# Performance work log

Measured on AMD Instinct MI355X. Metric: run time of the kernel, lower is better.

The kernel has to match this reference:

```python
import jax, jax.numpy as jnp
import numpy as np

N, E, D, H = 50000, 800000, 128, 8
HD = D // H
EPS = 1e-5


def _layernorm(x, w, b):
    # Custom LayerNorm from the repo: divides by (unbiased std + eps), not sqrt(var+eps)
    mu = x.mean(axis=-1, keepdims=True)
    sd = x.std(axis=-1, keepdims=True, ddof=1)
    return (x - mu) / (sd + EPS) * w + b


def setup_inputs() -> dict:
    key = jax.random.key(0)
    ks = jax.random.split(key, 16)
    s = 1.0 / np.sqrt(D)
    inp = {
        "feats": jax.random.normal(ks[0], (N, D), jnp.float32),
        "edge_index": jax.random.randint(ks[1], (E, 2), 0, N, jnp.int32),
        "Wq": jax.random.normal(ks[2], (D, D), jnp.float32) * s,
        "bq": jnp.zeros((D,), jnp.float32),
        "Wk": jax.random.normal(ks[3], (D, D), jnp.float32) * s,
        "bk": jnp.zeros((D,), jnp.float32),
        "Wv": jax.random.normal(ks[4], (D, D), jnp.float32) * s,
        "bv": jnp.zeros((D,), jnp.float32),
        "Wo": jax.random.normal(ks[5], (D, D), jnp.float32) * s,
        "bo": jnp.zeros((D,), jnp.float32),
        "ln1_w": jnp.ones((D,), jnp.float32),
        "ln1_b": jnp.zeros((D,), jnp.float32),
        "ln2_w": jnp.ones((D,), jnp.float32),
        "ln2_b": jnp.zeros((D,), jnp.float32),
        "W1": jax.random.normal(ks[6], (4 * D, D), jnp.float32) * s,
        "b1": jnp.zeros((4 * D,), jnp.float32),
        "W2": jax.random.normal(ks[7], (D, 4 * D), jnp.float32) * (1.0 / np.sqrt(4 * D)),
        "b2": jnp.zeros((D,), jnp.float32),
    }
    return inp


def reference(feats, edge_index, Wq, bq, Wk, bk, Wv, bv, Wo, bo,
              ln1_w, ln1_b, ln2_w, ln2_b, W1, b1, W2, b2):
    n = feats.shape[0]
    row, col = edge_index[:, 0], edge_index[:, 1]

    # --- multi-head dot-product attention over edges (dropout = identity, eval mode) ---
    x2 = _layernorm(feats, ln1_w, ln1_b)
    q = (x2 @ Wq.T + bq).reshape(n, H, HD)
    k = (x2 @ Wk.T + bk).reshape(n, H, HD)
    v = (x2 @ Wv.T + bv).reshape(n, H, HD)

    # per-edge scores: q[col] . k[row] / sqrt(head_dim)  -> [E, H]
    scores = jnp.einsum('ehd,ehd->eh', q[col], k[row]) / np.sqrt(HD).astype(np.float32)

    # scatter softmax normalized over groups of `row`
    smax = jax.ops.segment_max(scores, row, num_segments=n)       # [N, H]
    ex = jnp.exp(scores - smax[row])                              # [E, H]
    denom = jax.ops.segment_sum(ex, row, num_segments=n)         # [N, H]
    alpha = ex / denom[row]                                       # [E, H]

    # weighted messages, aggregated at col via scatter_add
    msg = alpha[:, :, None] * v[row]                              # [E, H, HD]
    agg = jax.ops.segment_sum(msg, col, num_segments=n).reshape(n, D)
    att = agg @ Wo.T + bo

    feats = feats + att  # residual 1

    # --- MLP block: note ReLU after BOTH linears (fc_dims=[4D, D], D != 1) ---
    x2 = _layernorm(feats, ln2_w, ln2_b)
    h = jax.nn.relu(x2 @ W1.T + b1)
    h = jax.nn.relu(h @ W2.T + b2)
    feats = feats + h  # residual 2
    return feats
```

## Files before the change

kernel.cpp:

```cpp
#include <hip/hip_runtime.h>
#include <hip/hip_bf16.h>
#include <math.h>

#define H_HEADS 8
constexpr float LN_EPS = 1e-5f;
constexpr int NBCH = 64;
constexpr int NSEG = 4;

using short8 = __attribute__((ext_vector_type(8))) short;
using f32x4  = __attribute__((ext_vector_type(4))) float;

__device__ __forceinline__ ushort f2bf(float v){
  __hip_bfloat16 h = __float2bfloat16(v);
  return *reinterpret_cast<ushort*>(&h);
}
__device__ __forceinline__ float bf2f(ushort u){
  return __uint_as_float(((unsigned)u) << 16);
}

__device__ __forceinline__ void stage16(const ushort* g, ushort* l){
  __builtin_amdgcn_global_load_lds((const __attribute__((address_space(1))) unsigned*)g,
                                   (__attribute__((address_space(3))) unsigned*)l,
                                   16, 0, 0);
}

__global__ void ln_kernel(const float* __restrict__ x, const float* __restrict__ w,
                          const float* __restrict__ b, ushort* __restrict__ out, int nrows){
  int wid = threadIdx.x >> 6, lane = threadIdx.x & 63;
  int r = blockIdx.x * (blockDim.x >> 6) + wid;
  if (r >= nrows) return;
  float2 v = ((const float2*)(x + (size_t)r*128))[lane];
  float s = v.x + v.y;
  #pragma unroll
  for (int o = 32; o; o >>= 1) s += __shfl_xor(s, o);
  float mu = s * (1.0f/128.0f);
  float d0 = v.x - mu, d1 = v.y - mu;
  float ss = d0*d0 + d1*d1;
  #pragma unroll
  for (int o = 32; o; o >>= 1) ss += __shfl_xor(ss, o);
  float sd = sqrtf(ss * (1.0f/127.0f));
  float inv = 1.0f / (sd + LN_EPS);
  float2 wv = ((const float2*)w)[lane];
  float2 bv = ((const float2*)b)[lane];
  ushort2 o2 = { f2bf(d0*inv*wv.x + bv.x), f2bf(d1*inv*wv.y + bv.y) };
  ((ushort2*)(out + (size_t)r*128))[lane] = o2;
}

struct CvtArgs { const float* s[6]; ushort* d[6]; int cnt[6]; };
__global__ void cvt6_kernel(CvtArgs a){
  int w = blockIdx.y;
  int i = blockIdx.x*blockDim.x + threadIdx.x;
  if (i < a.cnt[w]) a.d[w][i] = f2bf(a.s[w][i]);
}

template<int K, int RELU, int RESID, int OUT_BF16>
__device__ __forceinline__ void gemm_lds_body(
    const ushort* __restrict__ A, const ushort* __restrict__ W,
    const float* __restrict__ bias, const float* __restrict__ resid,
    void* __restrict__ out, int M, int Nout, int cb, ushort* Wl){
  constexpr int NCH = K / 128;
  int t = threadIdx.x;
  int wid = t >> 6, lane = t & 63;
  int mb = blockIdx.x * 64 + wid * 16;
  int lrow = lane & 15, kgrp = lane >> 4;
  int row = mb + lrow;
  bool rowok = row < M;
  const ushort* arow = A + (size_t)(rowok ? row : (M-1)) * K + kgrp*8;

  f32x4 acc[8] = {};
  short8 af[2][4];

  #pragma unroll
  for (int p = 0; p < 8; ++p){
    int L = p*256 + t;
    int colp = L >> 4, sp = L & 15;
    stage16(W + (size_t)colp*K + ((sp ^ (colp & 7)) << 3),
            (ushort*)((char*)Wl + ((size_t)(p*256 + (t & ~63)))*16));
  }
  #pragma unroll
  for (int kk = 0; kk < 4; ++kk)
    af[0][kk] = *(const short8*)(arow + kk*32);

  #pragma unroll
  for (int ci = 0; ci < NCH; ++ci){
    __syncthreads();
    int cur = ci & 1;
    if (ci + 1 < NCH){
      #pragma unroll
      for (int kk = 0; kk < 4; ++kk)
        af[cur^1][kk] = *(const short8*)(arow + (ci+1)*128 + kk*32);
    }
    #pragma unroll
    for (int kk = 0; kk < 4; ++kk){
      #pragma unroll
      for (int nt = 0; nt < 8; ++nt){
        int colc = nt*16 + lrow;
        int g = kk*4 + kgrp;
        short8 bfv = *(const short8*)((const char*)Wl + colc*256 + ((g ^ (colc & 7))*16));
        acc[nt] = __builtin_amdgcn_mfma_f32_16x16x32_bf16(af[cur][kk], bfv, acc[nt], 0, 0, 0);
      }
    }
    if (ci + 1 < NCH){
      __syncthreads();
      const ushort* Wc = W + (ci+1)*128;
      #pragma unroll
      for (int p = 0; p < 8; ++p){
        int L = p*256 + t;
        int colp = L >> 4, sp = L & 15;
        stage16(Wc + (size_t)colp*K + ((sp ^ (colp & 7)) << 3),
                (ushort*)((char*)Wl + ((size_t)(p*256 + (t & ~63)))*16));
      }
    }
  }

  int r0 = mb + kgrp*4;
  #pragma unroll
  for (int nt = 0; nt < 8; ++nt){
    int c = cb + nt*16 + lrow;
    float bsum = bias[c];
    #pragma unroll
    for (int i = 0; i < 4; ++i){
      int r = r0 + i;
      if (r >= M) continue;
      float v = acc[nt][i] + bsum;
      if (RELU)  v = fmaxf(v, 0.0f);
      if (RESID) v += resid[(size_t)r*Nout + c];
      if (OUT_BF16) ((ushort*)out)[(size_t)r*Nout + c] = f2bf(v);
      else          ((float*)out)[(size_t)r*Nout + c] = v;
    }
  }
}

template<int K, int RELU, int RESID, int OUT_BF16>
__global__ __launch_bounds__(256) void gemm_lds(
    const ushort* __restrict__ A, const ushort* __restrict__ Wfull,
    const float* __restrict__ bias, const float* __restrict__ resid,
    void* __restrict__ out, int M, int Nout){
  __shared__ __align__(16) ushort Wl[16384];
  int cb = blockIdx.y * 128;
  gemm_lds_body<K,RELU,RESID,OUT_BF16>(A, Wfull + (size_t)cb*K, bias, resid, out, M, Nout, cb, Wl);
}

__global__ __launch_bounds__(256) void qkv_lds(
    const ushort* __restrict__ A, const ushort* __restrict__ Wcat,
    const float* __restrict__ bq, const float* __restrict__ bk, const float* __restrict__ bv,
    ushort* __restrict__ qb, ushort* __restrict__ kb, ushort* __restrict__ vb, int M){
  __shared__ __align__(16) ushort Wl[16384];
  int y = blockIdx.y;
  const float* bias = (y==0) ? bq : (y==1) ? bk : bv;
  ushort* out = (y==0) ? qb : (y==1) ? kb : vb;
  gemm_lds_body<128,0,0,1>(A, Wcat + (size_t)y*16384, bias, nullptr, out, M, 128, 0, Wl);
}

__global__ __launch_bounds__(256) void hist_seg(const int* __restrict__ ei,
    unsigned* __restrict__ copies, int E, int n, int nw, int chunk, int nsb){
  __shared__ unsigned hh[8192];
  int b = blockIdx.x, s = blockIdx.y, y = blockIdx.z, t = threadIdx.x;
  int bin0 = s * nsb;
  int bin1 = min(bin0 + nsb, n);
  int words = (bin1 - bin0 + 1) >> 1;
  for (int i = t; i < words; i += 256) hh[i] = 0;
  __syncthreads();
  int lo = b*chunk, hi = min(lo + chunk, E);
  for (int e = lo + t; e < hi; e += 256){
    int2 rc = ((const int2*)ei)[e];
    int bin = y ? rc.y : rc.x;
    if (bin >= bin0 && bin < bin1)
      atomicAdd(&hh[(bin - bin0) >> 1], 1u << ((bin & 1)*16));
  }
  __syncthreads();
  unsigned* dst = copies + ((size_t)y*NBCH + b)*nw + (bin0 >> 1);
  for (int i = t; i < words; i += 256) dst[i] = hh[i];
}

__global__ __launch_bounds__(256) void scan_fold(const unsigned* __restrict__ copies,
    int* __restrict__ cnt2, int* __restrict__ choff, int n, int nw){
  int y = blockIdx.y;
  int bin = blockIdx.x*256 + threadIdx.x;
  if (bin >= n) return;
  const unsigned* cp = copies + (size_t)y*NBCH*nw + (bin >> 1);
  int sh = (bin & 1)*16;
  int run = 0;
  for (int b = 0; b < NBCH; ++b){
    int c = (int)((cp[(size_t)b*nw] >> sh) & 0xffffu);
    choff[((size_t)y*NBCH + b)*n + bin] = run;
    run += c;
  }
  cnt2[(size_t)y*n + bin] = run;
}

__global__ __launch_bounds__(256) void scan_reduce(const int* __restrict__ cnt0,
                                                   int* __restrict__ partial, int n, int nb){
  const int* cnt = cnt0 + (size_t)blockIdx.y * n;
  int t = threadIdx.x;
  int base = blockIdx.x*1024 + t*4;
  int s = 0;
  #pragma unroll
  for (int j = 0; j < 4; ++j){ int i = base+j; if (i < n) s += cnt[i]; }
  __shared__ int sm[256];
  sm[t] = s; __syncthreads();
  for (int off = 128; off; off >>= 1){
    if (t < off) sm[t] += sm[t+off];
    __syncthreads();
  }
  if (t == 0) partial[blockIdx.y*nb + blockIdx.x] = sm[0];
}

__global__ __launch_bounds__(256) void scan_mid(int* __restrict__ partial, int nb,
                                                int* __restrict__ rptr, int* __restrict__ cptr, int n){
  int y = blockIdx.y;
  int* p = partial + y*nb;
  int t = threadIdx.x;
  __shared__ int sm[256];
  sm[t] = (t < nb) ? p[t] : 0;
  __syncthreads();
  for (int off = 1; off < 256; off <<= 1){
    int v = (t >= off) ? sm[t-off] : 0;
    __syncthreads();
    sm[t] += v;
    __syncthreads();
  }
  if (t < nb) p[t] = (t == 0) ? 0 : sm[t-1];
  if (t == 0) (y ? cptr : rptr)[n] = sm[255];
}

__global__ __launch_bounds__(256) void scan_scatter(const int* __restrict__ cnt0,
                                                    const int* __restrict__ partial,
                                                    int* __restrict__ rptr, int* __restrict__ cptr,
                                                    int n, int nb){
  int y = blockIdx.y;
  const int* cnt = cnt0 + (size_t)y * n;
  int* ptr = y ? cptr : rptr;
  int t = threadIdx.x;
  int base = blockIdx.x*1024 + t*4;
  int v[4]; int s = 0;
  #pragma unroll
  for (int j = 0; j < 4; ++j){ int i = base+j; v[j] = (i<n)?cnt[i]:0; s += v[j]; }
  __shared__ int sm[256];
  sm[t] = s; __syncthreads();
  for (int off = 1; off < 256; off <<= 1){
    int x = (t >= off) ? sm[t-off] : 0;
    __syncthreads();
    sm[t] += x;
    __syncthreads();
  }
  int pre = partial[y*nb + blockIdx.x] + ((t==0)?0:sm[t-1]);
  #pragma unroll
  for (int j = 0; j < 4; ++j){
    int i = base+j;
    if (i < n){ ptr[i] = pre; pre += v[j]; }
  }
}

__global__ __launch_bounds__(256) void fill_r_seg(const int* __restrict__ ei,
    const int* __restrict__ rptr, const int* __restrict__ choffR,
    int* __restrict__ rcol, int* __restrict__ pose, int E, int n, int chunk, int nsb){
  __shared__ unsigned hh[8192];
  int b = blockIdx.x, s = blockIdx.y, t = threadIdx.x;
  int bin0 = s * nsb;
  int bin1 = min(bin0 + nsb, n);
  int words = (bin1 - bin0 + 1) >> 1;
  for (int i = t; i < words; i += 256) hh[i] = 0;
  __syncthreads();
  const int* chb = choffR + (size_t)b*n;
  int lo = b*chunk, hi = min(lo + chunk, E);
  for (int e = lo + t; e < hi; e += 256){
    int2 rc = ((const int2*)ei)[e];
    int bin = rc.x;
    if (bin < bin0 || bin >= bin1) continue;
    int sh = (bin & 1)*16;
    unsigned old = atomicAdd(&hh[(bin - bin0) >> 1], 1u << sh);
    int rank = (int)((old >> sh) & 0xffffu);
    int pos = rptr[bin] + chb[bin] + rank;
    rcol[pos] = rc.y;
    pose[e] = pos;
  }
}

__global__ __launch_bounds__(256) void fill_c_seg(const int* __restrict__ ei,
    const int* __restrict__ cptr, const int* __restrict__ choffC,
    const int* __restrict__ pose, int* __restrict__ crow, int* __restrict__ cposr,
    int E, int n, int chunk, int nsb){
  __shared__ unsigned hh[8192];
  int b = blockIdx.x, s = blockIdx.y, t = threadIdx.x;
  int bin0 = s * nsb;
  int bin1 = min(bin0 + nsb, n);
  int words = (bin1 - bin0 + 1) >> 1;
  for (int i = t; i < words; i += 256) hh[i] = 0;
  __syncthreads();
  const int* chb = choffC + (size_t)b*n;
  int lo = b*chunk, hi = min(lo + chunk, E);
  for (int e = lo + t; e < hi; e += 256){
    int2 rc = ((const int2*)ei)[e];
    int bin = rc.y;
    if (bin < bin0 || bin >= bin1) continue;
    int sh = (bin & 1)*16;
    unsigned old = atomicAdd(&hh[(bin - bin0) >> 1], 1u << sh);
    int rank = (int)((old >> sh) & 0xffffu);
    int pos = cptr[bin] + chb[bin] + rank;
    crow[pos] = rc.x;
    cposr[pose[e]] = pos;
  }
}

__device__ __forceinline__ float qdot16(const ushort* __restrict__ qb, int c, int h,
                                        const float kf[16]){
  const short8* qp = (const short8*)(qb + (size_t)c*128 + h*16);
  short8 q0 = qp[0], q1 = qp[1];
  float s = 0.f;
  #pragma unroll
  for (int i = 0; i < 8; ++i){
    s += bf2f((ushort)q0[i]) * kf[i];
    s += bf2f((ushort)q1[i]) * kf[8+i];
  }
  return s * 0.25f;
}

__global__ void row_softmax_kernel(const ushort* __restrict__ qb, const ushort* __restrict__ kb,
                                   const int* __restrict__ rptr, const int* __restrict__ rcol,
                                   const int* __restrict__ cposr,
                                   ushort* __restrict__ cbuf, int n){
  int wid = threadIdx.x >> 6, lane = threadIdx.x & 63;
  int r = blockIdx.x * (blockDim.x >> 6) + wid;
  if (r >= n) return;
  int lo = rptr[r], hi = rptr[r+1];
  if (lo >= hi) return;
  int h = lane & 7, el = lane >> 3;

  float kf[16];
  {
    const short8* kp = (const short8*)(kb + (size_t)r*128 + h*16);
    short8 k0 = kp[0], k1 = kp[1];
    #pragma unroll
    for (int i = 0; i < 8; ++i){
      kf[i]   = bf2f((ushort)k0[i]);
      kf[8+i] = bf2f((ushort)k1[i]);
    }
  }

  float m = -1e30f, d = 0.f;
  float sreg[8];
  #pragma unroll
  for (int ts = 0; ts < 8; ++ts){
    int j = lo + el + ts*8;
    float s = -1e30f;
    if (j < hi){
      s = qdot16(qb, rcol[j], h, kf);
      float nm = fmaxf(m, s);
      d = d*__expf(m - nm) + __expf(s - nm);
      m = nm;
    }
    sreg[ts] = s;
  }
  for (int j = lo + el + 64; j < hi; j += 8){
    float s = qdot16(qb, rcol[j], h, kf);
    float nm = fmaxf(m, s);
    d = d*__expf(m - nm) + __expf(s - nm);
    m = nm;
  }
  #pragma unroll
  for (int o = 8; o < 64; o <<= 1){
    float om = __shfl_xor(m, o);
    float od = __shfl_xor(d, o);
    float nm = fmaxf(m, om);
    d = d*__expf(m - nm) + od*__expf(om - nm);
    m = nm;
  }
  float invd = 1.0f / d;

  #pragma unroll
  for (int ts = 0; ts < 8; ++ts){
    int j = lo + el + ts*8;
    if (j < hi)
      cbuf[(size_t)cposr[j]*8 + h] = f2bf(__expf(sreg[ts] - m) * invd);
  }
  for (int j = lo + el + 64; j < hi; j += 8){
    float s = qdot16(qb, rcol[j], h, kf);
    cbuf[(size_t)cposr[j]*8 + h] = f2bf(__expf(s - m) * invd);
  }
}

__global__ void agg_kernel(const ushort* __restrict__ vb, const ushort* __restrict__ cbuf,
                           const int* __restrict__ cptr, const int* __restrict__ crow,
                           ushort* __restrict__ aggb, int n){
  int wid = threadIdx.x >> 6, lane = threadIdx.x & 63;
  int node = blockIdx.x * (blockDim.x >> 6) + wid;
  if (node >= n) return;
  int lo = cptr[node], hi = cptr[node+1];
  int qtr = lane >> 4, l16 = lane & 15;
  int h = l16 >> 1;
  float acc[8] = {};
  for (int j = lo + qtr; j < hi; j += 4){
    float a = bf2f(cbuf[(size_t)j*8 + h]);
    int row = crow[j];
    short8 vv = *(const short8*)(vb + (size_t)row*128 + l16*8);
    #pragma unroll
    for (int i = 0; i < 8; ++i)
      acc[i] = fmaf(a, bf2f((ushort)vv[i]), acc[i]);
  }
  #pragma unroll
  for (int i = 0; i < 8; ++i){
    acc[i] += __shfl_xor(acc[i], 16);
    acc[i] += __shfl_xor(acc[i], 32);
  }
  if (qtr == 0){
    short8 o8;
    #pragma unroll
    for (int i = 0; i < 8; ++i) o8[i] = (short)f2bf(acc[i]);
    *(short8*)(aggb + (size_t)node*128 + l16*8) = o8;
  }
}

extern "C" void kernel_launch(void* const* d_in, const int* in_sizes, int n_in,
                              void* d_out, int out_size, void* d_ws, size_t ws_size,
                              hipStream_t stream){
  const float* feats = (const float*)d_in[0];
  const int*   ei    = (const int*)  d_in[1];
  const float* Wq = (const float*)d_in[2];
  const float* bq = (const float*)d_in[3];
  const float* Wk = (const float*)d_in[4];
  const float* bk = (const float*)d_in[5];
  const float* Wv = (const float*)d_in[6];
  const float* bv = (const float*)d_in[7];
  const float* Wo = (const float*)d_in[8];
  const float* bo = (const float*)d_in[9];
  const float* ln1w = (const float*)d_in[10];
  const float* ln1b = (const float*)d_in[11];
  const float* ln2w = (const float*)d_in[12];
  const float* ln2b = (const float*)d_in[13];
  const float* W1 = (const float*)d_in[14];
  const float* b1 = (const float*)d_in[15];
  const float* W2 = (const float*)d_in[16];
  const float* b2 = (const float*)d_in[17];
  float* outp = (float*)d_out;

  int n = in_sizes[0] / 128;
  int E = in_sizes[1] / 2;
  int nw = (n + 1) >> 1;
  int chunk = (E + NBCH - 1) / NBCH;
  int nsb = (((n + NSEG - 1) / NSEG) + 1) & ~1;

  const size_t ND  = (size_t)n * 128;
  const size_t ND2 = ND / 2;
  const size_t EH  = (size_t)E * H_HEADS;

  float* ws = (float*)d_ws;
  ushort* x2b  = (ushort*)ws;
  ushort* qb   = (ushort*)(ws + ND2);
  ushort* kb   = (ushort*)(ws + 2*ND2);
  ushort* vb   = (ushort*)(ws + 3*ND2);
  ushort* cbuf = (ushort*)(ws + 4*ND2);
  ushort* aggb = (ushort*)(ws + 4*ND2 + EH/2);
  int* crow    = (int*)(ws + 5*ND2 + EH/2);
  int* cposr   = crow + E;
  int* rcol    = cposr + E;
  int* pose    = rcol + E;
  int* rptr    = pose + E;
  int* cptr    = rptr + (n + 4);
  int* cnt2    = cptr + (n + 4);
  int* choff   = cnt2 + 2*n;
  unsigned* copies = (unsigned*)(choff + (size_t)2*NBCH*n);
  int* partial = (int*)(copies + (size_t)2*NBCH*nw);
  ushort* wbuf = (ushort*)(partial + 512);
  ushort* Wqb = wbuf;
  ushort* Wkb = Wqb + 16384;
  ushort* Wvb = Wkb + 16384;
  ushort* Wob = Wvb + 16384;
  ushort* W1b = Wob + 16384;
  ushort* W2b = W1b + 65536;
  ushort* h1  = qb;

  CvtArgs ca;
  ca.s[0]=Wq; ca.s[1]=Wk; ca.s[2]=Wv; ca.s[3]=Wo; ca.s[4]=W1; ca.s[5]=W2;
  ca.d[0]=Wqb; ca.d[1]=Wkb; ca.d[2]=Wvb; ca.d[3]=Wob; ca.d[4]=W1b; ca.d[5]=W2b;
  ca.cnt[0]=ca.cnt[1]=ca.cnt[2]=ca.cnt[3]=16384; ca.cnt[4]=ca.cnt[5]=65536;
  cvt6_kernel<<<dim3(65536/256, 6), 256, 0, stream>>>(ca);

  int nb = (n + 1023)/1024;
  hist_seg  <<<dim3(NBCH,NSEG,2), 256, 0, stream>>>(ei, copies, E, n, nw, chunk, nsb);
  scan_fold <<<dim3((n+255)/256,2), 256, 0, stream>>>(copies, cnt2, choff, n, nw);
  scan_reduce <<<dim3(nb,2), 256, 0, stream>>>(cnt2, partial, n, nb);
  scan_mid    <<<dim3(1,2),  256, 0, stream>>>(partial, nb, rptr, cptr, n);
  scan_scatter<<<dim3(nb,2), 256, 0, stream>>>(cnt2, partial, rptr, cptr, n, nb);
  fill_r_seg<<<dim3(NBCH,NSEG), 256, 0, stream>>>(ei, rptr, choff,                  rcol, pose, E, n, chunk, nsb);
  fill_c_seg<<<dim3(NBCH,NSEG), 256, 0, stream>>>(ei, cptr, choff + (size_t)NBCH*n, pose, crow, cposr, E, n, chunk, nsb);

  ln_kernel<<<(n+3)/4, 256, 0, stream>>>(feats, ln1w, ln1b, x2b, n);

  int gm = (n + 63)/64;
  qkv_lds<<<dim3(gm,3), 256, 0, stream>>>(x2b, Wqb, bq, bk, bv, qb, kb, vb, n);

  row_softmax_kernel<<<(n+3)/4, 256, 0, stream>>>(qb, kb, rptr, rcol, cposr, cbuf, n);

  agg_kernel<<<(n+3)/4, 256, 0, stream>>>(vb, cbuf, cptr, crow, aggb, n);

  gemm_lds<128,0,1,0><<<dim3(gm,1), 256, 0, stream>>>(aggb, Wob, bo, feats, outp, n, 128);

  ln_kernel<<<(n+3)/4, 256, 0, stream>>>(outp, ln2w, ln2b, x2b, n);

  gemm_lds<128,1,0,1><<<dim3(gm,4), 256, 0, stream>>>(x2b, W1b, b1, nullptr, h1,  n, 512);
  gemm_lds<512,1,1,0><<<dim3(gm,1), 256, 0, stream>>>(h1,  W2b, b2, outp,    outp, n, 128);
}
```

Baseline: 315.8 us.

## Merge row/col histograms, use two-pass softmax, widen aggregation per-edge loads

The histogram kernel now counts both row and col bins in one pass over the edge list, using a doubled LDS array, instead of launching a z=2 grid that reads the edges twice. The row softmax replaces the online max/sum rescaling with a max pass and then a sum pass. This removes the per-edge rescaling exps but recomputes qdot for rows with more than 64 edges. The aggregation kernel now has each lane handle one head (16 values) with 8 edges in flight per wave instead of 4. That adds an extra shuffle stage and more registers.

```diff
diff --git a/kernel.cpp b/kernel.cpp
--- a/kernel.cpp
+++ b/kernel.cpp
@@ -152,25 +152,27 @@
   gemm_lds_body<128,0,0,1>(A, Wcat + (size_t)y*16384, bias, nullptr, out, M, 128, 0, Wl);
 }
 
-__global__ __launch_bounds__(256) void hist_seg(const int* __restrict__ ei,
+__global__ __launch_bounds__(256) void hist_seg2(const int* __restrict__ ei,
     unsigned* __restrict__ copies, int E, int n, int nw, int chunk, int nsb){
-  __shared__ unsigned hh[8192];
-  int b = blockIdx.x, s = blockIdx.y, y = blockIdx.z, t = threadIdx.x;
+  __shared__ unsigned hh[12544];
+  int b = blockIdx.x, s = blockIdx.y, t = threadIdx.x;
   int bin0 = s * nsb;
   int bin1 = min(bin0 + nsb, n);
   int words = (bin1 - bin0 + 1) >> 1;
-  for (int i = t; i < words; i += 256) hh[i] = 0;
+  for (int i = t; i < 2*words; i += 256) hh[i] = 0;
   __syncthreads();
   int lo = b*chunk, hi = min(lo + chunk, E);
   for (int e = lo + t; e < hi; e += 256){
     int2 rc = ((const int2*)ei)[e];
-    int bin = y ? rc.y : rc.x;
-    if (bin >= bin0 && bin < bin1)
-      atomicAdd(&hh[(bin - bin0) >> 1], 1u << ((bin & 1)*16));
+    if (rc.x >= bin0 && rc.x < bin1)
+      atomicAdd(&hh[(rc.x - bin0) >> 1], 1u << ((rc.x & 1)*16));
+    if (rc.y >= bin0 && rc.y < bin1)
+      atomicAdd(&hh[words + ((rc.y - bin0) >> 1)], 1u << ((rc.y & 1)*16));
   }
   __syncthreads();
-  unsigned* dst = copies + ((size_t)y*NBCH + b)*nw + (bin0 >> 1);
-  for (int i = t; i < words; i += 256) dst[i] = hh[i];
+  unsigned* d0 = copies + (size_t)b*nw + (bin0 >> 1);
+  unsigned* d1 = copies + (size_t)(NBCH + b)*nw + (bin0 >> 1);
+  for (int i = t; i < words; i += 256){ d0[i] = hh[i]; d1[i] = hh[words + i]; }
 }
 
 __global__ __launch_bounds__(256) void scan_fold(const unsigned* __restrict__ copies,
@@ -338,41 +340,36 @@
     }
   }
 
-  float m = -1e30f, d = 0.f;
   float sreg[8];
+  float m = -1e30f;
   #pragma unroll
   for (int ts = 0; ts < 8; ++ts){
     int j = lo + el + ts*8;
-    float s = -1e30f;
-    if (j < hi){
-      s = qdot16(qb, rcol[j], h, kf);
-      float nm = fmaxf(m, s);
-      d = d*__expf(m - nm) + __expf(s - nm);
-      m = nm;
-    }
+    float s = (j < hi) ? qdot16(qb, rcol[j], h, kf) : -1e30f;
     sreg[ts] = s;
-  }
-  for (int j = lo + el + 64; j < hi; j += 8){
-    float s = qdot16(qb, rcol[j], h, kf);
-    float nm = fmaxf(m, s);
-    d = d*__expf(m - nm) + __expf(s - nm);
-    m = nm;
-  }
-  #pragma unroll
-  for (int o = 8; o < 64; o <<= 1){
-    float om = __shfl_xor(m, o);
-    float od = __shfl_xor(d, o);
-    float nm = fmaxf(m, om);
-    d = d*__expf(m - nm) + od*__expf(om - nm);
-    m = nm;
-  }
-  float invd = 1.0f / d;
-
+    m = fmaxf(m, s);
+  }
+  for (int j = lo + el + 64; j < hi; j += 8)
+    m = fmaxf(m, qdot16(qb, rcol[j], h, kf));
+  #pragma unroll
+  for (int o = 8; o < 64; o <<= 1) m = fmaxf(m, __shfl_xor(m, o));
+
+  float d = 0.f;
   #pragma unroll
   for (int ts = 0; ts < 8; ++ts){
     int j = lo + el + ts*8;
-    if (j < hi)
-      cbuf[(size_t)cposr[j]*8 + h] = f2bf(__expf(sreg[ts] - m) * invd);
+    if (j < hi){ float e = __expf(sreg[ts] - m); sreg[ts] = e; d += e; }
+  }
+  for (int j = lo + el + 64; j < hi; j += 8)
+    d += __expf(qdot16(qb, rcol[j], h, kf) - m);
+  #pragma unroll
+  for (int o = 8; o < 64; o <<= 1) d += __shfl_xor(d, o);
+  float invd = 1.0f / d;
+
+  #pragma unroll
+  for (int ts = 0; ts < 8; ++ts){
+    int j = lo + el + ts*8;
+    if (j < hi) cbuf[(size_t)cposr[j]*8 + h] = f2bf(sreg[ts] * invd);
   }
   for (int j = lo + el + 64; j < hi; j += 8){
     float s = qdot16(qb, rcol[j], h, kf);
@@ -387,27 +384,31 @@
   int node = blockIdx.x * (blockDim.x >> 6) + wid;
   if (node >= n) return;
   int lo = cptr[node], hi = cptr[node+1];
-  int qtr = lane >> 4, l16 = lane & 15;
-  int h = l16 >> 1;
-  float acc[8] = {};
-  for (int j = lo + qtr; j < hi; j += 4){
-    float a = bf2f(cbuf[(size_t)j*8 + h]);
+  int oct = lane >> 3, l8 = lane & 7;
+  float acc[16] = {};
+  for (int j = lo + oct; j < hi; j += 8){
+    float a = bf2f(cbuf[(size_t)j*8 + l8]);
     int row = crow[j];
-    short8 vv = *(const short8*)(vb + (size_t)row*128 + l16*8);
+    const short8* vp = (const short8*)(vb + (size_t)row*128 + l8*16);
+    short8 v0 = vp[0], v1 = vp[1];
     #pragma unroll
-    for (int i = 0; i < 8; ++i)
-      acc[i] = fmaf(a, bf2f((ushort)vv[i]), acc[i]);
-  }
-  #pragma unroll
-  for (int i = 0; i < 8; ++i){
+    for (int i = 0; i < 8; ++i){
+      acc[i]   = fmaf(a, bf2f((ushort)v0[i]), acc[i]);
+      acc[8+i] = fmaf(a, bf2f((ushort)v1[i]), acc[8+i]);
+    }
+  }
+  #pragma unroll
+  for (int i = 0; i < 16; ++i){
+    acc[i] += __shfl_xor(acc[i], 8);
     acc[i] += __shfl_xor(acc[i], 16);
     acc[i] += __shfl_xor(acc[i], 32);
   }
-  if (qtr == 0){
-    short8 o8;
+  if (oct == 0){
+    short8 o0, o1;
     #pragma unroll
-    for (int i = 0; i < 8; ++i) o8[i] = (short)f2bf(acc[i]);
-    *(short8*)(aggb + (size_t)node*128 + l16*8) = o8;
+    for (int i = 0; i < 8; ++i){ o0[i] = (short)f2bf(acc[i]); o1[i] = (short)f2bf(acc[8+i]); }
+    short8* op = (short8*)(aggb + (size_t)node*128 + l8*16);
+    op[0] = o0; op[1] = o1;
   }
 }
 
@@ -477,7 +478,7 @@
   cvt6_kernel<<<dim3(65536/256, 6), 256, 0, stream>>>(ca);
 
   int nb = (n + 1023)/1024;
-  hist_seg  <<<dim3(NBCH,NSEG,2), 256, 0, stream>>>(ei, copies, E, n, nw, chunk, nsb);
+  hist_seg2 <<<dim3(NBCH,NSEG), 256, 0, stream>>>(ei, copies, E, n, nw, chunk, nsb);
   scan_fold <<<dim3((n+255)/256,2), 256, 0, stream>>>(copies, cnt2, choff, n, nw);
   scan_reduce <<<dim3(nb,2), 256, 0, stream>>>(cnt2, partial, n, nb);
   scan_mid    <<<dim3(1,2),  256, 0, stream>>>(partial, nb, rptr, cptr, n);
```

New measurement: 314.8 us. Within noise of the previous version (-0.3%).
